# Kernel tuning notes

Measured on AMD Instinct MI355X. Metric: run time of the kernel, lower is better.

The kernel has to match this reference:

```python
import jax, jax.numpy as jnp
import numpy as np

D_MODEL = 768
NUM_HEADS = 48
HEAD_CH = D_MODEL // NUM_HEADS  # 16
INNER = 3 * D_MODEL
BATCH = 2
SEQLEN = 2048
SKIP = 1.0
EPS = 1e-6


def setup_inputs() -> dict:
    key = jax.random.key(0)
    ks = jax.random.split(key, 9)
    s_in = 1.0 / np.sqrt(D_MODEL)
    s_out = 1.0 / np.sqrt(D_MODEL)
    return {
        "inputs": jax.random.normal(ks[0], (BATCH, SEQLEN, D_MODEL), jnp.float32),
        "w_in": jax.random.normal(ks[1], (INNER, D_MODEL), jnp.float32) * s_in,
        "b_in": jax.random.normal(ks[2], (INNER,), jnp.float32) * 0.01,
        "w_sf": jax.random.normal(ks[3], (INNER, 3), jnp.float32) * 0.3,  # depthwise conv kernel
        "b_sf": jax.random.normal(ks[4], (INNER,), jnp.float32) * 0.01,
        "h": jax.random.normal(ks[5], (NUM_HEADS, SEQLEN), jnp.float32) * 0.02,  # long filter
        "norm_w": jnp.ones((D_MODEL,), jnp.float32),
        "w_out": jax.random.normal(ks[6], (D_MODEL, D_MODEL), jnp.float32) * s_out,
        "b_out": jax.random.normal(ks[7], (D_MODEL,), jnp.float32) * 0.01,
    }


def reference(inputs, w_in, b_in, w_sf, b_sf, h, norm_w, w_out, b_out):
    B, L, D = inputs.shape
    N, HC = NUM_HEADS, HEAD_CH
    # in_proj: [B, L, 3D]
    u = jnp.einsum('bld,ed->ble', inputs, w_in) + b_in
    u = jnp.transpose(u, (0, 2, 1))  # [B, 3D, L]
    # causal depthwise conv1d, kernel 3, left pad 2
    up = jnp.pad(u, ((0, 0), (0, 0), (2, 0)))
    uc = (w_sf[:, 0:1] * up[:, :, 0:L]
          + w_sf[:, 1:2] * up[:, :, 1:L + 1]
          + w_sf[:, 2:3] * up[:, :, 2:L + 2]
          + b_sf[:, None])  # [B, 3D, L]
    uc = uc.reshape(B, N, 3 * HC, L)
    x0 = uc[:, :, 0:HC, :]            # q  [B, N, HC, L]
    x1 = uc[:, :, HC:2 * HC, :]       # k  [B, N, HC, L]
    v = uc[:, :, 2 * HC:3 * HC, :]    # v  [B, N, HC, L]
    # outer product: [B, HC_i, HC_j, N, L]
    kv = jnp.einsum('bnil,bnjl->bijnl', x1, v)
    # FFT long convolution with h [N, L], broadcast over b,i,j
    fft_size = 2 * L
    k_f = jnp.fft.rfft(h, n=fft_size) / fft_size        # [N, L+1]
    u_f = jnp.fft.rfft(kv, n=fft_size, axis=-1)         # [B, HC, HC, N, L+1]
    hkv = jnp.fft.irfft(u_f * k_f, n=fft_size, axis=-1, norm='forward')[..., :L]
    # contract with q: [B, L, N, HC_j]
    qhkv = jnp.einsum('bijnl,bnil->blnj', hkv, x0)
    y = qhkv.reshape(B, L, D)
    # RMSNorm
    ms = jnp.mean(jnp.square(y), axis=-1, keepdims=True)
    y = y * jax.lax.rsqrt(ms + EPS) * norm_w
    # out_proj + skip
    y = jnp.einsum('bld,ed->ble', y, w_out) + b_out
    return y + inputs * SKIP
```

## Files before the change

### kernel.cpp

```cpp
#include <hip/hip_runtime.h>
#include <hip/hip_bf16.h>
#include <stdint.h>

typedef __bf16 bf16;
typedef __bf16 bf16x4 __attribute__((ext_vector_type(4)));
typedef __bf16 bf16x8 __attribute__((ext_vector_type(8)));
typedef float f32x4 __attribute__((ext_vector_type(4)));
typedef float f32x16 __attribute__((ext_vector_type(16)));

#define D_MODEL 768
#define NUM_HEADS 48
#define HEAD_CH 16
#define INNER 2304
#define BATCH 2
#define SEQLEN 2048
#define M_ROWS (BATCH * SEQLEN)
#define EPSF 1e-6f
#define SST 40

__device__ inline void gload_lds16(const void* g, void* l) {
  __builtin_amdgcn_global_load_lds((__attribute__((address_space(1))) void*)(g),
                                   (__attribute__((address_space(3))) void*)(l),
                                   16, 0, 0);
}

__global__ __launch_bounds__(256) void cvt2_f32_bf16(
    const float* __restrict__ a, bf16* __restrict__ da, int na4,
    const float* __restrict__ b, bf16* __restrict__ db, int nb4) {
  int j = blockIdx.x * 256 + threadIdx.x;
  const float* s;
  bf16* d;
  if (j < na4) {
    s = a; d = da;
  } else {
    j -= na4;
    if (j >= nb4) return;
    s = b; d = db;
  }
  const float4 v = ((const float4*)s)[j];
  bf16x4 o;
  o[0] = (bf16)v.x; o[1] = (bf16)v.y; o[2] = (bf16)v.z; o[3] = (bf16)v.w;
  ((bf16x4*)d)[j] = o;
}

__global__ __launch_bounds__(256) void cvt_f32_bf16(
    const float* __restrict__ src, bf16* __restrict__ dst, int n4) {
  const int i = blockIdx.x * 256 + threadIdx.x;
  if (i < n4) {
    const float4 v = ((const float4*)src)[i];
    bf16x4 o;
    o[0] = (bf16)v.x; o[1] = (bf16)v.y; o[2] = (bf16)v.z; o[3] = (bf16)v.w;
    ((bf16x4*)dst)[i] = o;
  }
}

template <int TM, int TN, int BK, int NCOLS, bool ADD_SKIP, typename CT>
__global__ __launch_bounds__(256) void gemm_bt(
    const bf16* __restrict__ A, const bf16* __restrict__ W,
    const float* __restrict__ bias, const float* __restrict__ skip,
    CT* __restrict__ C, int K) {
  constexpr int MI = TM / 32;
  constexpr int NI = TN / 32;
  constexpr int KK = BK / 32;
  __shared__ __align__(16) bf16 As[TM * BK];
  __shared__ __align__(16) bf16 Bs[TN * BK];
  const int t = threadIdx.x;
  const int lane = t & 63, w = t >> 6;
  const int wm = (w >> 1) * (TM / 2), wn = (w & 1) * (TN / 2);
  const int row16 = lane & 15, quad = lane >> 4;
  const int m0 = blockIdx.x * TM, n0 = blockIdx.y * TN;

  f32x4 zero4 = {0.f, 0.f, 0.f, 0.f};
  f32x4 acc[MI][NI];
#pragma unroll
  for (int mi = 0; mi < MI; ++mi)
#pragma unroll
    for (int ni = 0; ni < NI; ++ni) acc[mi][ni] = zero4;

  const int arow = t >> 2;
  const int acol = (t & 3) * 8;
  const bf16* Ab = A + (size_t)m0 * K;
  const bf16* Wb = W + (size_t)n0 * K;

  for (int kt = 0; kt < K; kt += BK) {
#pragma unroll
    for (int kk0 = 0; kk0 < KK; ++kk0) {
#pragma unroll
      for (int rh = 0; rh < TM / 64; ++rh)
        gload_lds16(Ab + (size_t)(rh * 64 + arow) * K + kt + kk0 * 32 + acol,
                    As + kk0 * (TM * 32) + rh * 2048 + t * 8);
#pragma unroll
      for (int rh = 0; rh < TN / 64; ++rh)
        gload_lds16(Wb + (size_t)(rh * 64 + arow) * K + kt + kk0 * 32 + acol,
                    Bs + kk0 * (TN * 32) + rh * 2048 + t * 8);
    }
    __syncthreads();

    bf16x8 af[MI][KK], wf[NI][KK];
#pragma unroll
    for (int kk0 = 0; kk0 < KK; ++kk0) {
#pragma unroll
      for (int mi = 0; mi < MI; ++mi)
        af[mi][kk0] = *(const bf16x8*)&As[kk0 * (TM * 32) +
                                          (wm + mi * 16 + row16) * 32 +
                                          quad * 8];
#pragma unroll
      for (int ni = 0; ni < NI; ++ni)
        wf[ni][kk0] = *(const bf16x8*)&Bs[kk0 * (TN * 32) +
                                          (wn + ni * 16 + row16) * 32 +
                                          quad * 8];
    }
#pragma unroll
    for (int kk0 = 0; kk0 < KK; ++kk0)
#pragma unroll
      for (int mi = 0; mi < MI; ++mi)
#pragma unroll
        for (int ni = 0; ni < NI; ++ni)
          acc[mi][ni] = __builtin_amdgcn_mfma_f32_16x16x32_bf16(
              af[mi][kk0], wf[ni][kk0], acc[mi][ni], 0, 0, 0);
    __syncthreads();
  }

#pragma unroll
  for (int mi = 0; mi < MI; ++mi) {
#pragma unroll
    for (int ni = 0; ni < NI; ++ni) {
      const int col = n0 + wn + ni * 16 + row16;
      const float bv = bias[col];
#pragma unroll
      for (int r = 0; r < 4; ++r) {
        const int row = m0 + wm + mi * 16 + quad * 4 + r;
        float v = acc[mi][ni][r] + bv;
        if (ADD_SKIP) v += skip[(size_t)row * NCOLS + col];
        C[(size_t)row * NCOLS + col] = (CT)v;
      }
    }
  }
}

__global__ __launch_bounds__(256) void conv_qkv(
    const bf16* __restrict__ u, const float* __restrict__ w_sf,
    const float* __restrict__ b_sf, bf16* __restrict__ qq,
    bf16* __restrict__ kk, bf16* __restrict__ vv) {
  const int nh = blockIdx.x, b = blockIdx.y, lc = blockIdx.z;
  const int l0 = lc * 128;
  __shared__ __align__(8) bf16 ut[130 * 48];
  const int t = threadIdx.x;
  for (int i = t; i < 130 * 12; i += 256) {
    const int lr = i / 12, qd = i % 12;
    const int l = l0 - 2 + lr;
    uint2 val;
    val.x = 0u; val.y = 0u;
    if (l >= 0)
      val = *(const uint2*)&u[(size_t)(b * SEQLEN + l) * INNER + nh * 48 + qd * 4];
    *(uint2*)&ut[lr * 48 + qd * 4] = val;
  }
  __syncthreads();
  const size_t bn = (size_t)(b * NUM_HEADS + nh);
#pragma unroll
  for (int s = 0; s < 2; ++s) {
    bf16* dst = (s == 0) ? qq : kk;
    const int cb = s * 16;
    for (int i = t; i < 128 * 16; i += 256) {
      const int c = i & 15, lr = i >> 4;
      const int e = nh * 48 + cb + c;
      const float val = w_sf[e * 3 + 0] * (float)ut[lr * 48 + cb + c] +
                        w_sf[e * 3 + 1] * (float)ut[(lr + 1) * 48 + cb + c] +
                        w_sf[e * 3 + 2] * (float)ut[(lr + 2) * 48 + cb + c] +
                        b_sf[e];
      dst[(bn * SEQLEN + l0 + lr) * 16 + c] = (bf16)val;
    }
  }
  for (int i = t; i < 128 * 16; i += 256) {
    const int lr = i & 127, c = i >> 7;
    const int e = nh * 48 + 32 + c;
    const float val = w_sf[e * 3 + 0] * (float)ut[lr * 48 + 32 + c] +
                      w_sf[e * 3 + 1] * (float)ut[(lr + 1) * 48 + 32 + c] +
                      w_sf[e * 3 + 2] * (float)ut[(lr + 2) * 48 + 32 + c] +
                      b_sf[e];
    vv[(bn * 16 + c) * SEQLEN + l0 + lr] = (bf16)val;
  }
}

__global__ __launch_bounds__(256) void attn_kernel(
    const bf16* __restrict__ qq, const bf16* __restrict__ kk,
    const bf16* __restrict__ vv, const float* __restrict__ hg,
    bf16* __restrict__ y) {
  const int nh = blockIdx.x, b = blockIdx.y;
  const int qa = blockIdx.z, qb = 63 - qa;
  const int l0a = qa * 32, l0b = qb * 32;
  __shared__ __align__(16) float hs[32 + SEQLEN];
  __shared__ __align__(16) bf16 st[4 * 32 * SST];
  const int t = threadIdx.x;
  const int n4 = (l0b + 64) >> 2;
  for (int i = t; i < n4; i += 256) {
    float4 val = {0.f, 0.f, 0.f, 0.f};
    if (i >= 8) val = ((const float4*)(hg + nh * SEQLEN))[i - 8];
    ((float4*)hs)[i] = val;
  }
  __syncthreads();

  const int w = t >> 6, lane = t & 63;
  const int l31 = lane & 31, hi = lane >> 5;
  const int row16 = lane & 15, quad = lane >> 4;
  const size_t bn = (size_t)(b * NUM_HEADS + nh);
  const bf16* qp = qq + bn * SEQLEN * 16;
  const bf16* kb = kk + bn * SEQLEN * 16;
  const bf16* vb = vv + bn * 16 * SEQLEN;

  bf16x8 zf;
#pragma unroll
  for (int j = 0; j < 8; ++j) zf[j] = (bf16)0.f;
  const f32x4 zacc4 = {0.f, 0.f, 0.f, 0.f};
  f32x16 zacc16;
#pragma unroll
  for (int j = 0; j < 16; ++j) zacc16[j] = 0.f;

  const bf16x8 qfa = *(const bf16x8*)&qp[(l0a + l31) * 16 + hi * 8];
  const bf16x8 qfb = *(const bf16x8*)&qp[(l0b + l31) * 16 + hi * 8];

  bf16* sw = &st[w * 32 * SST];

  auto run_pass = [&](const bf16x8& qf, const int l0, const int mc0,
                      f32x4& o0, f32x4& o1) {
    int mc = mc0;
    bf16x8 kf = zf, vf = zf;
    if (mc <= l0) {
      kf = *(const bf16x8*)&kb[(mc + l31) * 16 + hi * 8];
      vf = *(const bf16x8*)&vb[row16 * SEQLEN + mc + quad * 8];
    }
    for (; mc <= l0; mc += 128) {
      const int mn = mc + 128;
      bf16x8 kf2 = zf, vf2 = zf;
      if (mn <= l0) {
        kf2 = *(const bf16x8*)&kb[(mn + l31) * 16 + hi * 8];
        vf2 = *(const bf16x8*)&vb[row16 * SEQLEN + mn + quad * 8];
      }
      f32x16 s =
          __builtin_amdgcn_mfma_f32_32x32x16_bf16(kf, qf, zacc16, 0, 0, 0);

      const int d0 = 32 + (l0 - mc) + l31 - 4 * hi;
#pragma unroll
      for (int g = 0; g < 4; ++g) {
        const float* hp = &hs[d0 - 8 * g - 3];
        bf16x4 pk;
        pk[0] = (bf16)(s[4 * g + 0] * hp[3]);
        pk[1] = (bf16)(s[4 * g + 1] * hp[2]);
        pk[2] = (bf16)(s[4 * g + 2] * hp[1]);
        pk[3] = (bf16)(s[4 * g + 3] * hp[0]);
        *(bf16x4*)&sw[l31 * SST + 8 * g + 4 * hi] = pk;
      }
      asm volatile("s_waitcnt lgkmcnt(0)" ::: "memory");
      const bf16x8 sf0 = *(const bf16x8*)&sw[row16 * SST + quad * 8];
      const bf16x8 sf1 = *(const bf16x8*)&sw[(row16 + 16) * SST + quad * 8];
      o0 = __builtin_amdgcn_mfma_f32_16x16x32_bf16(sf0, vf, o0, 0, 0, 0);
      o1 = __builtin_amdgcn_mfma_f32_16x16x32_bf16(sf1, vf, o1, 0, 0, 0);
      asm volatile("" ::: "memory");
      kf = kf2; vf = vf2;
    }
  };

  f32x4 o0a = zacc4, o1a = zacc4, o0b = zacc4, o1b = zacc4;
  run_pass(qfa, l0a, w * 32, o0a, o1a);
  const int j0 = ((w - qa - 1) % 4 + 4) % 4;
  run_pass(qfb, l0b, j0 * 32, o0b, o1b);

  float* ob = (float*)&st[w * 32 * SST];
#pragma unroll
  for (int phase = 0; phase < 2; ++phase) {
    const f32x4& p0 = phase ? o0b : o0a;
    const f32x4& p1 = phase ? o1b : o1a;
    const int lt = phase ? l0b : l0a;
    __syncthreads();
#pragma unroll
    for (int r = 0; r < 4; ++r) {
      ob[(quad * 4 + r) * 16 + row16] = p0[r];
      ob[(quad * 4 + r + 16) * 16 + row16] = p1[r];
    }
    __syncthreads();
    for (int i = t; i < 32 * 16; i += 256) {
      const int l = i >> 4, j = i & 15;
      float sum = 0.f;
#pragma unroll
      for (int ww = 0; ww < 4; ++ww)
        sum += ((const float*)&st[ww * 32 * SST])[l * 16 + j];
      y[((size_t)(b * SEQLEN + lt + l) * NUM_HEADS + nh) * 16 + j] = (bf16)sum;
    }
  }
}

__global__ __launch_bounds__(256) void rmsnorm_k(
    const bf16* __restrict__ y, const float* __restrict__ nw,
    bf16* __restrict__ yn) {
  const int row = blockIdx.x;
  const int t = threadIdx.x;
  const bf16* yr = y + (size_t)row * D_MODEL;
  const float v0 = (float)yr[t];
  const float v1 = (float)yr[t + 256];
  const float v2 = (float)yr[t + 512];
  float ss = v0 * v0 + v1 * v1 + v2 * v2;
#pragma unroll
  for (int off = 32; off >= 1; off >>= 1) ss += __shfl_down(ss, off, 64);
  __shared__ float red[4];
  if ((t & 63) == 0) red[t >> 6] = ss;
  __syncthreads();
  const float tot = red[0] + red[1] + red[2] + red[3];
  const float r = rsqrtf(tot * (1.f / 768.f) + EPSF);
  bf16* yo = yn + (size_t)row * D_MODEL;
  yo[t] = (bf16)(v0 * r * nw[t]);
  yo[t + 256] = (bf16)(v1 * r * nw[t + 256]);
  yo[t + 512] = (bf16)(v2 * r * nw[t + 512]);
}

extern "C" void kernel_launch(void* const* d_in, const int* in_sizes, int n_in,
                              void* d_out, int out_size, void* d_ws,
                              size_t ws_size, hipStream_t stream) {
  const float* inputs = (const float*)d_in[0];
  const float* w_in = (const float*)d_in[1];
  const float* b_in = (const float*)d_in[2];
  const float* w_sf = (const float*)d_in[3];
  const float* b_sf = (const float*)d_in[4];
  const float* hb = (const float*)d_in[5];
  const float* norm_w = (const float*)d_in[6];
  const float* w_out = (const float*)d_in[7];
  const float* b_out = (const float*)d_in[8];

  char* ws = (char*)d_ws;
  const size_t U_B = (size_t)M_ROWS * INNER * 2;
  const size_t V_B = (size_t)BATCH * NUM_HEADS * HEAD_CH * SEQLEN * 2;
  const size_t SLOT_B = (size_t)M_ROWS * D_MODEL * 2;
  bf16* u = (bf16*)(ws);
  bf16* wout16 = (bf16*)(ws);
  bf16* yn = (bf16*)(ws + (2 << 20));
  bf16* y16 = (bf16*)(ws + (9 << 20));
  bf16* v = (bf16*)(ws + U_B);
  bf16* in16 = (bf16*)(ws + U_B + V_B);
  bf16* k16 = in16;
  bf16* win16 = (bf16*)(ws + U_B + V_B + SLOT_B);
  bf16* q16 = win16;
  float* out = (float*)d_out;

  const int n4_in = M_ROWS * D_MODEL / 4;
  const int n4_win = INNER * D_MODEL / 4;
  const int n4_wout = D_MODEL * D_MODEL / 4;
  hipLaunchKernelGGL(cvt2_f32_bf16, dim3((n4_in + n4_win + 255) / 256),
                     dim3(256), 0, stream, inputs, in16, n4_in, w_in, win16,
                     n4_win);

  hipLaunchKernelGGL((gemm_bt<128, 128, 64, INNER, false, bf16>), dim3(32, 18),
                     dim3(256), 0, stream, in16, win16, b_in,
                     (const float*)nullptr, u, 768);
  hipLaunchKernelGGL(conv_qkv, dim3(48, 2, 16), dim3(256), 0, stream, u, w_sf,
                     b_sf, q16, k16, v);
  hipLaunchKernelGGL(cvt_f32_bf16, dim3((n4_wout + 255) / 256), dim3(256), 0,
                     stream, w_out, wout16, n4_wout);
  hipLaunchKernelGGL(attn_kernel, dim3(48, 2, 32), dim3(256), 0, stream, q16,
                     k16, v, hb, y16);
  hipLaunchKernelGGL(rmsnorm_k, dim3(M_ROWS), dim3(256), 0, stream, y16,
                     norm_w, yn);
  hipLaunchKernelGGL((gemm_bt<64, 64, 64, D_MODEL, true, float>), dim3(64, 12),
                     dim3(256), 0, stream, yn, wout16, b_out, inputs, out,
                     768);
}
```

Measured before the change: 185.3 us.

## Fuse RMSNorm into out-proj GEMM, precompute bf16 Toeplitz filter table, vectorize conv

Removes the separate RMSNorm kernel by folding norm_w into the bf16 w_out conversion and computing per-row sum of squares inside the out-projection GEMM from the A tiles in LDS, then scaling the accumulators. The long filter h is pre-expanded into a bf16 table laid out to match the MFMA score-fragment registers, so attention loads filter values directly from global memory with prefetch instead of staging h in LDS and syncing. The depthwise conv kernel is vectorized to 4-wide loads and stores. In exchange, the sum of squares is taken over bf16-rounded y, and the filter table adds extra workspace traffic.

```diff
diff --git a/kernel.cpp b/kernel.cpp
--- a/kernel.cpp
+++ b/kernel.cpp
@@ -17,6 +17,8 @@
 #define M_ROWS (BATCH * SEQLEN)
 #define EPSF 1e-6f
 #define SST 40
+#define HT_ROWS 2052
+#define HTQ (NUM_HEADS * HT_ROWS * 4)
 
 __device__ inline void gload_lds16(const void* g, void* l) {
   __builtin_amdgcn_global_load_lds((__attribute__((address_space(1))) void*)(g),
@@ -43,22 +45,41 @@
   ((bf16x4*)d)[j] = o;
 }
 
-__global__ __launch_bounds__(256) void cvt_f32_bf16(
-    const float* __restrict__ src, bf16* __restrict__ dst, int n4) {
-  const int i = blockIdx.x * 256 + threadIdx.x;
-  if (i < n4) {
-    const float4 v = ((const float4*)src)[i];
+__global__ __launch_bounds__(256) void cvt_wout_hgen(
+    const float* __restrict__ wout, const float* __restrict__ nw,
+    bf16* __restrict__ wout16, int n4, const float* __restrict__ hb,
+    bf16* __restrict__ ht) {
+  int j = blockIdx.x * 256 + threadIdx.x;
+  if (j < n4) {
+    const int d0 = (j * 4) % D_MODEL;
+    const float4 v = ((const float4*)wout)[j];
+    const float4 nv = *(const float4*)&nw[d0];
     bf16x4 o;
-    o[0] = (bf16)v.x; o[1] = (bf16)v.y; o[2] = (bf16)v.z; o[3] = (bf16)v.w;
-    ((bf16x4*)dst)[i] = o;
-  }
-}
-
-template <int TM, int TN, int BK, int NCOLS, bool ADD_SKIP, typename CT>
+    o[0] = (bf16)(v.x * nv.x); o[1] = (bf16)(v.y * nv.y);
+    o[2] = (bf16)(v.z * nv.z); o[3] = (bf16)(v.w * nv.w);
+    ((bf16x4*)wout16)[j] = o;
+    return;
+  }
+  j -= n4;
+  if (j >= HTQ) return;
+  const int nh = j / (HT_ROWS * 4);
+  const int rem = j - nh * (HT_ROWS * 4);
+  const int Cp = rem >> 2, rb = rem & 3;
+  const float* hrow = hb + nh * SEQLEN;
+  const int base = Cp - 4 - 8 * rb;
+  bf16x4 o;
+#pragma unroll
+  for (int rr = 0; rr < 4; ++rr) {
+    const int idx = base - rr;
+    o[rr] = (bf16)((idx >= 0 && idx < SEQLEN) ? hrow[idx] : 0.f);
+  }
+  ((bf16x4*)ht)[j] = o;
+}
+
+template <int TM, int TN, int BK, int NCOLS, typename CT>
 __global__ __launch_bounds__(256) void gemm_bt(
     const bf16* __restrict__ A, const bf16* __restrict__ W,
-    const float* __restrict__ bias, const float* __restrict__ skip,
-    CT* __restrict__ C, int K) {
+    const float* __restrict__ bias, CT* __restrict__ C, int K) {
   constexpr int MI = TM / 32;
   constexpr int NI = TN / 32;
   constexpr int KK = BK / 32;
@@ -130,9 +151,106 @@
 #pragma unroll
       for (int r = 0; r < 4; ++r) {
         const int row = m0 + wm + mi * 16 + quad * 4 + r;
-        float v = acc[mi][ni][r] + bv;
-        if (ADD_SKIP) v += skip[(size_t)row * NCOLS + col];
-        C[(size_t)row * NCOLS + col] = (CT)v;
+        C[(size_t)row * NCOLS + col] = (CT)(acc[mi][ni][r] + bv);
+      }
+    }
+  }
+}
+
+__global__ __launch_bounds__(256) void gemm_rms(
+    const bf16* __restrict__ A, const bf16* __restrict__ W,
+    const float* __restrict__ bias, const float* __restrict__ skip,
+    float* __restrict__ C) {
+  constexpr int TM = 64, TN = 64, BK = 64, K = D_MODEL;
+  constexpr int MI = 2, NI = 2, KK = 2;
+  __shared__ __align__(16) bf16 As[TM * BK];
+  __shared__ __align__(16) bf16 Bs[TN * BK];
+  __shared__ float rs[TM];
+  const int t = threadIdx.x;
+  const int lane = t & 63, w = t >> 6;
+  const int wm = (w >> 1) * 32, wn = (w & 1) * 32;
+  const int row16 = lane & 15, quad = lane >> 4;
+  const int m0 = blockIdx.x * TM, n0 = blockIdx.y * TN;
+
+  f32x4 zero4 = {0.f, 0.f, 0.f, 0.f};
+  f32x4 acc[MI][NI];
+#pragma unroll
+  for (int mi = 0; mi < MI; ++mi)
+#pragma unroll
+    for (int ni = 0; ni < NI; ++ni) acc[mi][ni] = zero4;
+
+  const int arow = t >> 2;
+  const int acol = (t & 3) * 8;
+  const bf16* Ab = A + (size_t)m0 * K;
+  const bf16* Wb = W + (size_t)n0 * K;
+  float ssq = 0.f;
+
+  for (int kt = 0; kt < K; kt += BK) {
+#pragma unroll
+    for (int kk0 = 0; kk0 < KK; ++kk0) {
+      gload_lds16(Ab + (size_t)arow * K + kt + kk0 * 32 + acol,
+                  As + kk0 * (TM * 32) + t * 8);
+      gload_lds16(Wb + (size_t)arow * K + kt + kk0 * 32 + acol,
+                  Bs + kk0 * (TN * 32) + t * 8);
+    }
+    __syncthreads();
+
+    bf16x8 af[MI][KK], wf[NI][KK];
+#pragma unroll
+    for (int kk0 = 0; kk0 < KK; ++kk0) {
+#pragma unroll
+      for (int mi = 0; mi < MI; ++mi)
+        af[mi][kk0] = *(const bf16x8*)&As[kk0 * (TM * 32) +
+                                          (wm + mi * 16 + row16) * 32 +
+                                          quad * 8];
+#pragma unroll
+      for (int ni = 0; ni < NI; ++ni)
+        wf[ni][kk0] = *(const bf16x8*)&Bs[kk0 * (TN * 32) +
+                                          (wn + ni * 16 + row16) * 32 +
+                                          quad * 8];
+    }
+#pragma unroll
+    for (int kk0 = 0; kk0 < KK; ++kk0) {
+      const bf16x8 q =
+          *(const bf16x8*)&As[kk0 * (TM * 32) + (t >> 2) * 32 + (t & 3) * 8];
+#pragma unroll
+      for (int jj = 0; jj < 8; ++jj) {
+        const float f = (float)q[jj];
+        ssq += f * f;
+      }
+    }
+#pragma unroll
+    for (int kk0 = 0; kk0 < KK; ++kk0)
+#pragma unroll
+      for (int mi = 0; mi < MI; ++mi)
+#pragma unroll
+        for (int ni = 0; ni < NI; ++ni)
+          acc[mi][ni] = __builtin_amdgcn_mfma_f32_16x16x32_bf16(
+              af[mi][kk0], wf[ni][kk0], acc[mi][ni], 0, 0, 0);
+    __syncthreads();
+  }
+
+  float* ssr = (float*)As;
+  ssr[t] = ssq;
+  __syncthreads();
+  if (t < TM) {
+    const float s4 = ssr[4 * t] + ssr[4 * t + 1] + ssr[4 * t + 2] + ssr[4 * t + 3];
+    rs[t] = rsqrtf(s4 * (1.f / (float)D_MODEL) + EPSF);
+  }
+  __syncthreads();
+
+#pragma unroll
+  for (int mi = 0; mi < MI; ++mi) {
+#pragma unroll
+    for (int ni = 0; ni < NI; ++ni) {
+      const int col = n0 + wn + ni * 16 + row16;
+      const float bv = bias[col];
+#pragma unroll
+      for (int r = 0; r < 4; ++r) {
+        const int rowl = wm + mi * 16 + quad * 4 + r;
+        const int row = m0 + rowl;
+        C[(size_t)row * D_MODEL + col] =
+            acc[mi][ni][r] * rs[rowl] + bv + skip[(size_t)row * D_MODEL + col];
       }
     }
   }
@@ -161,45 +279,53 @@
   for (int s = 0; s < 2; ++s) {
     bf16* dst = (s == 0) ? qq : kk;
     const int cb = s * 16;
-    for (int i = t; i < 128 * 16; i += 256) {
-      const int c = i & 15, lr = i >> 4;
-      const int e = nh * 48 + cb + c;
-      const float val = w_sf[e * 3 + 0] * (float)ut[lr * 48 + cb + c] +
-                        w_sf[e * 3 + 1] * (float)ut[(lr + 1) * 48 + cb + c] +
-                        w_sf[e * 3 + 2] * (float)ut[(lr + 2) * 48 + cb + c] +
-                        b_sf[e];
-      dst[(bn * SEQLEN + l0 + lr) * 16 + c] = (bf16)val;
-    }
-  }
-  for (int i = t; i < 128 * 16; i += 256) {
-    const int lr = i & 127, c = i >> 7;
+    for (int i = t; i < 128 * 4; i += 256) {
+      const int c4 = (i & 3) * 4, lr = i >> 2;
+      const int e0 = nh * 48 + cb + c4;
+      const float4 wa = *(const float4*)&w_sf[e0 * 3];
+      const float4 wb = *(const float4*)&w_sf[e0 * 3 + 4];
+      const float4 wc = *(const float4*)&w_sf[e0 * 3 + 8];
+      const float4 bb = *(const float4*)&b_sf[e0];
+      const bf16x4 u0 = *(const bf16x4*)&ut[lr * 48 + cb + c4];
+      const bf16x4 u1 = *(const bf16x4*)&ut[(lr + 1) * 48 + cb + c4];
+      const bf16x4 u2 = *(const bf16x4*)&ut[(lr + 2) * 48 + cb + c4];
+      bf16x4 o;
+      o[0] = (bf16)(wa.x * (float)u0[0] + wa.y * (float)u1[0] +
+                    wa.z * (float)u2[0] + bb.x);
+      o[1] = (bf16)(wa.w * (float)u0[1] + wb.x * (float)u1[1] +
+                    wb.y * (float)u2[1] + bb.y);
+      o[2] = (bf16)(wb.z * (float)u0[2] + wb.w * (float)u1[2] +
+                    wc.x * (float)u2[2] + bb.z);
+      o[3] = (bf16)(wc.y * (float)u0[3] + wc.z * (float)u1[3] +
+                    wc.w * (float)u2[3] + bb.w);
+      *(bf16x4*)&dst[(bn * SEQLEN + l0 + lr) * 16 + c4] = o;
+    }
+  }
+  for (int i = t; i < 16 * 32; i += 256) {
+    const int c = i >> 5, lr4 = (i & 31) * 4;
     const int e = nh * 48 + 32 + c;
-    const float val = w_sf[e * 3 + 0] * (float)ut[lr * 48 + 32 + c] +
-                      w_sf[e * 3 + 1] * (float)ut[(lr + 1) * 48 + 32 + c] +
-                      w_sf[e * 3 + 2] * (float)ut[(lr + 2) * 48 + 32 + c] +
-                      b_sf[e];
-    vv[(bn * 16 + c) * SEQLEN + l0 + lr] = (bf16)val;
+    const float w0 = w_sf[e * 3 + 0], w1 = w_sf[e * 3 + 1],
+                w2 = w_sf[e * 3 + 2], bv = b_sf[e];
+    bf16x4 o;
+#pragma unroll
+    for (int k = 0; k < 4; ++k) {
+      o[k] = (bf16)(w0 * (float)ut[(lr4 + k) * 48 + 32 + c] +
+                    w1 * (float)ut[(lr4 + k + 1) * 48 + 32 + c] +
+                    w2 * (float)ut[(lr4 + k + 2) * 48 + 32 + c] + bv);
+    }
+    *(bf16x4*)&vv[(bn * 16 + c) * SEQLEN + l0 + lr4] = o;
   }
 }
 
 __global__ __launch_bounds__(256) void attn_kernel(
     const bf16* __restrict__ qq, const bf16* __restrict__ kk,
-    const bf16* __restrict__ vv, const float* __restrict__ hg,
+    const bf16* __restrict__ vv, const bf16* __restrict__ ht,
     bf16* __restrict__ y) {
   const int nh = blockIdx.x, b = blockIdx.y;
   const int qa = blockIdx.z, qb = 63 - qa;
   const int l0a = qa * 32, l0b = qb * 32;
-  __shared__ __align__(16) float hs[32 + SEQLEN];
   __shared__ __align__(16) bf16 st[4 * 32 * SST];
   const int t = threadIdx.x;
-  const int n4 = (l0b + 64) >> 2;
-  for (int i = t; i < n4; i += 256) {
-    float4 val = {0.f, 0.f, 0.f, 0.f};
-    if (i >= 8) val = ((const float4*)(hg + nh * SEQLEN))[i - 8];
-    ((float4*)hs)[i] = val;
-  }
-  __syncthreads();
-
   const int w = t >> 6, lane = t & 63;
   const int l31 = lane & 31, hi = lane >> 5;
   const int row16 = lane & 15, quad = lane >> 4;
@@ -207,6 +333,7 @@
   const bf16* qp = qq + bn * SEQLEN * 16;
   const bf16* kb = kk + bn * SEQLEN * 16;
   const bf16* vb = vv + bn * 16 * SEQLEN;
+  const bf16* hbase = ht + ((size_t)nh * HT_ROWS + (size_t)(l31 - 4 * hi + 4)) * 16;
 
   bf16x8 zf;
 #pragma unroll
@@ -224,30 +351,36 @@
   auto run_pass = [&](const bf16x8& qf, const int l0, const int mc0,
                       f32x4& o0, f32x4& o1) {
     int mc = mc0;
-    bf16x8 kf = zf, vf = zf;
+    bf16x8 kf = zf, vf = zf, hf0 = zf, hf1 = zf;
     if (mc <= l0) {
       kf = *(const bf16x8*)&kb[(mc + l31) * 16 + hi * 8];
       vf = *(const bf16x8*)&vb[row16 * SEQLEN + mc + quad * 8];
+      const bf16* hp = hbase + (size_t)(l0 - mc) * 16;
+      hf0 = *(const bf16x8*)hp;
+      hf1 = *(const bf16x8*)(hp + 8);
     }
     for (; mc <= l0; mc += 128) {
       const int mn = mc + 128;
-      bf16x8 kf2 = zf, vf2 = zf;
+      bf16x8 kf2 = zf, vf2 = zf, hn0 = zf, hn1 = zf;
       if (mn <= l0) {
         kf2 = *(const bf16x8*)&kb[(mn + l31) * 16 + hi * 8];
         vf2 = *(const bf16x8*)&vb[row16 * SEQLEN + mn + quad * 8];
+        const bf16* hp = hbase + (size_t)(l0 - mn) * 16;
+        hn0 = *(const bf16x8*)hp;
+        hn1 = *(const bf16x8*)(hp + 8);
       }
       f32x16 s =
           __builtin_amdgcn_mfma_f32_32x32x16_bf16(kf, qf, zacc16, 0, 0, 0);
 
-      const int d0 = 32 + (l0 - mc) + l31 - 4 * hi;
 #pragma unroll
       for (int g = 0; g < 4; ++g) {
-        const float* hp = &hs[d0 - 8 * g - 3];
         bf16x4 pk;
-        pk[0] = (bf16)(s[4 * g + 0] * hp[3]);
-        pk[1] = (bf16)(s[4 * g + 1] * hp[2]);
-        pk[2] = (bf16)(s[4 * g + 2] * hp[1]);
-        pk[3] = (bf16)(s[4 * g + 3] * hp[0]);
+#pragma unroll
+        for (int r = 0; r < 4; ++r) {
+          const int reg = 4 * g + r;
+          const float hv = (float)((g < 2) ? hf0[reg] : hf1[reg - 8]);
+          pk[r] = (bf16)(s[reg] * hv);
+        }
         *(bf16x4*)&sw[l31 * SST + 8 * g + 4 * hi] = pk;
       }
       asm volatile("s_waitcnt lgkmcnt(0)" ::: "memory");
@@ -256,7 +389,7 @@
       o0 = __builtin_amdgcn_mfma_f32_16x16x32_bf16(sf0, vf, o0, 0, 0, 0);
       o1 = __builtin_amdgcn_mfma_f32_16x16x32_bf16(sf1, vf, o1, 0, 0, 0);
       asm volatile("" ::: "memory");
-      kf = kf2; vf = vf2;
+      kf = kf2; vf = vf2; hf0 = hn0; hf1 = hn1;
     }
   };
 
@@ -287,29 +420,6 @@
       y[((size_t)(b * SEQLEN + lt + l) * NUM_HEADS + nh) * 16 + j] = (bf16)sum;
     }
   }
-}
-
-__global__ __launch_bounds__(256) void rmsnorm_k(
-    const bf16* __restrict__ y, const float* __restrict__ nw,
-    bf16* __restrict__ yn) {
-  const int row = blockIdx.x;
-  const int t = threadIdx.x;
-  const bf16* yr = y + (size_t)row * D_MODEL;
-  const float v0 = (float)yr[t];
-  const float v1 = (float)yr[t + 256];
-  const float v2 = (float)yr[t + 512];
-  float ss = v0 * v0 + v1 * v1 + v2 * v2;
-#pragma unroll
-  for (int off = 32; off >= 1; off >>= 1) ss += __shfl_down(ss, off, 64);
-  __shared__ float red[4];
-  if ((t & 63) == 0) red[t >> 6] = ss;
-  __syncthreads();
-  const float tot = red[0] + red[1] + red[2] + red[3];
-  const float r = rsqrtf(tot * (1.f / 768.f) + EPSF);
-  bf16* yo = yn + (size_t)row * D_MODEL;
-  yo[t] = (bf16)(v0 * r * nw[t]);
-  yo[t + 256] = (bf16)(v1 * r * nw[t + 256]);
-  yo[t + 512] = (bf16)(v2 * r * nw[t + 512]);
 }
 
 extern "C" void kernel_launch(void* const* d_in, const int* in_sizes, int n_in,
@@ -331,7 +441,7 @@
   const size_t SLOT_B = (size_t)M_ROWS * D_MODEL * 2;
   bf16* u = (bf16*)(ws);
   bf16* wout16 = (bf16*)(ws);
-  bf16* yn = (bf16*)(ws + (2 << 20));
+  bf16* ht = (bf16*)(ws + (2 << 20));
   bf16* y16 = (bf16*)(ws + (9 << 20));
   bf16* v = (bf16*)(ws + U_B);
   bf16* in16 = (bf16*)(ws + U_B + V_B);
@@ -347,18 +457,15 @@
                      dim3(256), 0, stream, inputs, in16, n4_in, w_in, win16,
                      n4_win);
 
-  hipLaunchKernelGGL((gemm_bt<128, 128, 64, INNER, false, bf16>), dim3(32, 18),
-                     dim3(256), 0, stream, in16, win16, b_in,
-                     (const float*)nullptr, u, 768);
+  hipLaunchKernelGGL((gemm_bt<128, 128, 64, INNER, bf16>), dim3(32, 18),
+                     dim3(256), 0, stream, in16, win16, b_in, u, 768);
   hipLaunchKernelGGL(conv_qkv, dim3(48, 2, 16), dim3(256), 0, stream, u, w_sf,
                      b_sf, q16, k16, v);
-  hipLaunchKernelGGL(cvt_f32_bf16, dim3((n4_wout + 255) / 256), dim3(256), 0,
-                     stream, w_out, wout16, n4_wout);
+  hipLaunchKernelGGL(cvt_wout_hgen, dim3((n4_wout + HTQ + 255) / 256),
+                     dim3(256), 0, stream, w_out, norm_w, wout16, n4_wout, hb,
+                     ht);
   hipLaunchKernelGGL(attn_kernel, dim3(48, 2, 32), dim3(256), 0, stream, q16,
-                     k16, v, hb, y16);
-  hipLaunchKernelGGL(rmsnorm_k, dim3(M_ROWS), dim3(256), 0, stream, y16,
-                     norm_w, yn);
-  hipLaunchKernelGGL((gemm_bt<64, 64, 64, D_MODEL, true, float>), dim3(64, 12),
-                     dim3(256), 0, stream, yn, wout16, b_out, inputs, out,
-                     768);
-}
+                     k16, v, ht, y16);
+  hipLaunchKernelGGL(gemm_rms, dim3(64, 12), dim3(256), 0, stream, y16, wout16,
+                     b_out, inputs, out);
+}
```

New measurement: 192.6 us. 3.9% more time.
